# Optimization experiments

Hardware: AMD Instinct MI355X
Metric: run time of the kernel (lower is better)

The kernel has to match this reference:

```python
import jax, jax.numpy as jnp
import numpy as np

N_NODES, N_EDGES, F_IN, F_OUT = 10000, 320000, 256, 256


def setup_inputs() -> dict:
    key = jax.random.key(0)
    k1, k2, k3, k4, k5, k6 = jax.random.split(key, 6)
    feature = jax.random.normal(k1, (N_NODES, F_IN), jnp.float32)
    ew = jax.random.uniform(k2, (N_EDGES,), jnp.float32)          # edge weights
    src = jax.random.randint(k3, (N_EDGES,), 0, N_NODES)
    dst = jax.random.randint(k4, (N_EDGES,), 0, N_NODES)
    # nn.Linear(2*in_feats, out_feats): weight [out, 2*in], bias [out]
    W = jax.random.normal(k5, (F_OUT, 2 * F_IN), jnp.float32) / np.sqrt(2 * F_IN)
    b = jax.random.normal(k6, (F_OUT,), jnp.float32) * 0.01
    return {"feature": feature, "ew": ew, "src": src, "dst": dst, "W": W, "b": b}


def reference(feature, ew, src, dst, W, b):
    n = feature.shape[0]
    # edge_msg2: m[e] = h[src[0]] * h[src[e]] * w[e]   -> [E, F]
    msg = feature[src[0]] * feature[src] * ew[:, None]
    # reduce: segment mean over incoming edges (mailbox mean). The original
    # reduce also computes a segment max concatenated into 'hm', but the apply
    # module only consumes the mean half ('hm_mean', Linear in = 2*in_feats),
    # so the max is dead compute and omitted.
    sums = jax.ops.segment_sum(msg, dst, num_segments=n)
    cnt = jax.ops.segment_sum(jnp.ones((msg.shape[0],), msg.dtype), dst, num_segments=n)
    hm_mean = sums / jnp.maximum(cnt, 1.0)[:, None]
    # NodeApplyModule: relu(Linear(cat(h, hm_mean)))
    x = jnp.concatenate([feature, hm_mean], axis=1)  # [N, 2F]
    return jax.nn.relu(x @ W.T + b)
```

## Files before the change

### kernel.cpp

```cpp
#include <hip/hip_runtime.h>

#define N_NODES 10000
#define N_EDGES 320000
#define F 256
#define K2 512
#define HSLOT 48
#define SLOTS 96
#define CSTR 16
#define W_BLOCKS 128
#define ZCNT_BLOCKS 313
#define K0_BLOCKS (W_BLOCKS + ZCNT_BLOCKS)
#define K1_BLOCKS 4375
#define N_TILE16 625

typedef __attribute__((ext_vector_type(8))) __bf16 bf16x8;
typedef __attribute__((ext_vector_type(4))) __bf16 bf16x4;
typedef __attribute__((ext_vector_type(4))) float f32x4;
typedef __attribute__((ext_vector_type(2))) float f32x2;
typedef unsigned long long u64;
typedef unsigned int u32;
typedef unsigned short u16;


__global__ __launch_bounds__(256) void prep_kernel(
    const float* __restrict__ feat,
    const float* __restrict__ Wm,
    const int* __restrict__ src,
    __bf16* __restrict__ Wt,
    int* __restrict__ cnt) {
  int b = blockIdx.x;
  int tid = threadIdx.x;
  if (b < W_BLOCKS) {
    int idx = b * 256 + tid;
    int o_ = idx >> 7;
    int k = (idx & 127) * 4;
    float4 w = ((const float4*)Wm)[idx];
    if (k >= F) {
      int s0 = src[0];
      float4 h = ((const float4*)(feat + (size_t)s0 * F))[(k - F) >> 2];
      w.x *= h.x; w.y *= h.y; w.z *= h.z; w.w *= h.w;
    }
    bf16x4 o;
    o[0] = (__bf16)w.x; o[1] = (__bf16)w.y; o[2] = (__bf16)w.z; o[3] = (__bf16)w.w;
    int t = k >> 5, kq = (k & 31) >> 3, e = k & 7;
    size_t offT = (((size_t)t * 4 + kq) * 256 + o_) * 8 + e;
    *(bf16x4*)(Wt + offT) = o;
  } else {
    int idx = (b - W_BLOCKS) * 256 + tid;
    if (idx < 2 * N_NODES * CSTR / 4) ((int4*)cnt)[idx] = make_int4(0, 0, 0, 0);
  }
}

__global__ __launch_bounds__(256) void mega_kernel(
    const float* __restrict__ feat,
    const int* __restrict__ src,
    const int* __restrict__ dst,
    const float* __restrict__ ew,
    int* __restrict__ cnt,
    u32* __restrict__ bucket,
    u32* __restrict__ feat8,
    const __bf16* __restrict__ Wt,
    const float* __restrict__ bias,
    float* __restrict__ out) {
  int b = blockIdx.x;
  int tid = threadIdx.x;
  int g = b / 7;
  int r = b % 7;
  if (r == 0 || r == 3) {
    int sid = g * 2 + (r == 3);
    int e = sid * 256 + tid;
    if (e >= N_EDGES) return;
    int d = dst[e];
    int par = e & 1;
    u32 wb = (__float_as_uint(ew[e]) + 0x8000u) & 0xFFFF0000u;
    int p = atomicAdd(&cnt[(d * 2 + par) * CSTR], 1);
    if (p < HSLOT) bucket[(size_t)d * SLOTS + par * HSLOT + p] = wb | (u32)src[e];
  } else if (r == 6) {
    int mt = g;
    const int wave = tid >> 6;
    const int lane = tid & 63;
    const int r15 = lane & 15;
    const int kq = lane >> 4;
    const int col0 = wave * 64;
    const int m0 = mt * 16;
    const float* arow = feat + (size_t)(m0 + r15) * F;

    f32x4 acc[4];
#pragma unroll
    for (int cs = 0; cs < 4; ++cs) acc[cs] = (f32x4){0.f, 0.f, 0.f, 0.f};

#pragma unroll
    for (int t = 0; t < 8; ++t) {
      float4 lo = *(const float4*)(arow + t * 32 + kq * 8);
      float4 hi = *(const float4*)(arow + t * 32 + kq * 8 + 4);
      bf16x8 a;
      a[0] = (__bf16)lo.x; a[1] = (__bf16)lo.y; a[2] = (__bf16)lo.z; a[3] = (__bf16)lo.w;
      a[4] = (__bf16)hi.x; a[5] = (__bf16)hi.y; a[6] = (__bf16)hi.z; a[7] = (__bf16)hi.w;
#pragma unroll
      for (int cs = 0; cs < 4; ++cs) {
        bf16x8 bb = *(const bf16x8*)(Wt + (((size_t)t * 4 + kq) * 256 + col0 + cs * 16 + r15) * 8);
        acc[cs] = __builtin_amdgcn_mfma_f32_16x16x32_bf16(a, bb, acc[cs], 0, 0, 0);
      }
    }

    const int rbase = kq * 4;
#pragma unroll
    for (int cs = 0; cs < 4; ++cs) {
      int col = col0 + cs * 16 + r15;
      float bv = bias[col];
#pragma unroll
      for (int r2 = 0; r2 < 4; ++r2) {
        int orow = m0 + rbase + r2;
        out[(size_t)orow * F + col] = acc[cs][r2] + bv;
      }
    }
  } else {
    int ci = (r < 3) ? (r - 1) : (r - 2);
    int idx = (g * 4 + ci) * 256 + tid;
    float4 v = ((const float4*)feat)[idx];
    u32 r8 = 0;
    r8 = __builtin_amdgcn_cvt_pk_fp8_f32(v.x, v.y, r8, false);
    r8 = __builtin_amdgcn_cvt_pk_fp8_f32(v.z, v.w, r8, true);
    feat8[idx] = r8;
  }
}

__global__ __launch_bounds__(256) void node_agg_kernel(
    const u32* __restrict__ feat8,
    const u32* __restrict__ bucket,
    const int* __restrict__ cnt,
    __bf16* __restrict__ aggb) {
  int node = (blockIdx.x * 256 + threadIdx.x) >> 6;
  int lane = threadIdx.x & 63;
  if (node >= N_NODES) return;
  int c0 = cnt[(node * 2) * CSTR];
  int c1 = cnt[(node * 2 + 1) * CSTR];
  int cc0 = min(c0, HSLOT);
  int cc1 = min(c1, HSLOT);
  int cc = cc0 + cc1;
  int c = c0 + c1;
  const u32* bk = bucket + (size_t)node * SLOTS;
  const uint2* frow = (const uint2*)feat8;
  const int half = lane >> 5;
  const int slot = lane & 31;

  float acc[8];
#pragma unroll
  for (int e = 0; e < 8; ++e) acc[e] = 0.f;

  for (int i = 0; i < cc; i += 16) {
    u32 p[8];
    uint2 v[8];
#pragma unroll
    for (int j = 0; j < 8; ++j) {
      int e = i + half + 2 * j;
      int ec = min(e, cc - 1);
      int si = (ec < cc0) ? ec : (ec - cc0 + HSLOT);
      p[j] = bk[si];
    }
#pragma unroll
    for (int j = 0; j < 8; ++j)
      v[j] = frow[(size_t)(p[j] & 0xFFFFu) * 32 + slot];
#pragma unroll
    for (int j = 0; j < 8; ++j) {
      int e = i + half + 2 * j;
      float w = (e < cc) ? __uint_as_float(p[j] & 0xFFFF0000u) : 0.f;
      f32x2 f01 = __builtin_amdgcn_cvt_pk_f32_fp8(v[j].x, false);
      f32x2 f23 = __builtin_amdgcn_cvt_pk_f32_fp8(v[j].x, true);
      f32x2 f45 = __builtin_amdgcn_cvt_pk_f32_fp8(v[j].y, false);
      f32x2 f67 = __builtin_amdgcn_cvt_pk_f32_fp8(v[j].y, true);
      acc[0] += f01[0] * w; acc[1] += f01[1] * w;
      acc[2] += f23[0] * w; acc[3] += f23[1] * w;
      acc[4] += f45[0] * w; acc[5] += f45[1] * w;
      acc[6] += f67[0] * w; acc[7] += f67[1] * w;
    }
  }

#pragma unroll
  for (int e = 0; e < 8; ++e) acc[e] += __shfl_xor(acc[e], 32, 64);

  if (half == 0) {
    float ic = 1.0f / (float)max(c, 1);
    bf16x8 o;
#pragma unroll
    for (int e = 0; e < 8; ++e) o[e] = (__bf16)(acc[e] * ic);
    *(bf16x8*)(aggb + (size_t)node * F + slot * 8) = o;
  }
}

__global__ __launch_bounds__(256) void gemmB_kernel(
    const __bf16* __restrict__ aggb,
    const __bf16* __restrict__ Wt,
    float* __restrict__ out) {
  const int tid = threadIdx.x;
  const int wave = tid >> 6;
  const int lane = tid & 63;
  const int r15 = lane & 15;
  const int kq = lane >> 4;
  const int col0 = wave * 64;
  const int m0 = blockIdx.x * 16;

  const __bf16* arow = aggb + (size_t)(m0 + r15) * F;

  f32x4 acc[4];
#pragma unroll
  for (int cs = 0; cs < 4; ++cs) acc[cs] = (f32x4){0.f, 0.f, 0.f, 0.f};

#pragma unroll
  for (int t2 = 0; t2 < 8; ++t2) {
    bf16x8 a = *(const bf16x8*)(arow + t2 * 32 + kq * 8);
#pragma unroll
    for (int cs = 0; cs < 4; ++cs) {
      bf16x8 bb = *(const bf16x8*)(Wt + (((size_t)(t2 + 8) * 4 + kq) * 256 + col0 + cs * 16 + r15) * 8);
      acc[cs] = __builtin_amdgcn_mfma_f32_16x16x32_bf16(a, bb, acc[cs], 0, 0, 0);
    }
  }

  const int rbase = kq * 4;
#pragma unroll
  for (int cs = 0; cs < 4; ++cs) {
    int col = col0 + cs * 16 + r15;
#pragma unroll
    for (int r = 0; r < 4; ++r) {
      int orow = m0 + rbase + r;
      size_t oi = (size_t)orow * F + col;
      out[oi] = fmaxf(out[oi] + acc[cs][r], 0.0f);
    }
  }
}

extern "C" void kernel_launch(void* const* d_in, const int* in_sizes, int n_in,
                              void* d_out, int out_size, void* d_ws, size_t ws_size,
                              hipStream_t stream) {
  const float* feat = (const float*)d_in[0];
  const float* ew   = (const float*)d_in[1];
  const int*   src  = (const int*)d_in[2];
  const int*   dst  = (const int*)d_in[3];
  const float* Wm   = (const float*)d_in[4];
  const float* bias = (const float*)d_in[5];
  float* out = (float*)d_out;

  u32*    bucket = (u32*)d_ws;
  __bf16* aggb   = (__bf16*)(bucket + (size_t)N_NODES * SLOTS);
  __bf16* Wt     = aggb + (size_t)N_NODES * F;
  u32*    feat8  = (u32*)(Wt + (size_t)F * K2);
  int*    cnt    = (int*)(feat8 + (size_t)N_NODES * F / 4);

  prep_kernel<<<K0_BLOCKS, 256, 0, stream>>>(feat, Wm, src, Wt, cnt);
  mega_kernel<<<K1_BLOCKS, 256, 0, stream>>>(feat, src, dst, ew, cnt, bucket,
                                             feat8, Wt, bias, out);
  node_agg_kernel<<<(N_NODES * 64 + 255) / 256, 256, 0, stream>>>(feat8, bucket, cnt, aggb);
  gemmB_kernel<<<N_TILE16, 256, 0, stream>>>(aggb, Wt, out);
}
```

Before: 54.50 us.

## Fuse node aggregation into second GEMM via shared-memory tile

Merges the per-node gather/mean kernel with the second-half GEMM: each block aggregates its 16 nodes (4 per wave) into an LDS tile, then runs the MFMA GEMM directly from LDS. This removes one kernel launch and the global round trip of the bf16 aggregate buffer. In exchange, the aggregation now runs on only 625 blocks with each wave handling 4 nodes serially, which lowers parallelism and latency hiding for the gather phase.

```diff
diff --git a/kernel.cpp b/kernel.cpp
--- a/kernel.cpp
+++ b/kernel.cpp
@@ -12,6 +12,7 @@
 #define K0_BLOCKS (W_BLOCKS + ZCNT_BLOCKS)
 #define K1_BLOCKS 4375
 #define N_TILE16 625
+#define LDSROW 264
 
 typedef __attribute__((ext_vector_type(8))) __bf16 bf16x8;
 typedef __attribute__((ext_vector_type(4))) __bf16 bf16x4;
@@ -125,82 +126,80 @@
   }
 }
 
-__global__ __launch_bounds__(256) void node_agg_kernel(
+__global__ __launch_bounds__(256) void aggB_kernel(
     const u32* __restrict__ feat8,
     const u32* __restrict__ bucket,
     const int* __restrict__ cnt,
-    __bf16* __restrict__ aggb) {
-  int node = (blockIdx.x * 256 + threadIdx.x) >> 6;
-  int lane = threadIdx.x & 63;
-  if (node >= N_NODES) return;
-  int c0 = cnt[(node * 2) * CSTR];
-  int c1 = cnt[(node * 2 + 1) * CSTR];
-  int cc0 = min(c0, HSLOT);
-  int cc1 = min(c1, HSLOT);
-  int cc = cc0 + cc1;
-  int c = c0 + c1;
-  const u32* bk = bucket + (size_t)node * SLOTS;
+    const __bf16* __restrict__ Wt,
+    float* __restrict__ out) {
+  __shared__ __bf16 aggs[16][LDSROW];
+
+  const int tid = threadIdx.x;
+  const int wave = tid >> 6;
+  const int lane = tid & 63;
+  const int m0 = blockIdx.x * 16;
+
   const uint2* frow = (const uint2*)feat8;
   const int half = lane >> 5;
   const int slot = lane & 31;
-
-  float acc[8];
-#pragma unroll
-  for (int e = 0; e < 8; ++e) acc[e] = 0.f;
-
-  for (int i = 0; i < cc; i += 16) {
-    u32 p[8];
-    uint2 v[8];
-#pragma unroll
-    for (int j = 0; j < 8; ++j) {
-      int e = i + half + 2 * j;
-      int ec = min(e, cc - 1);
-      int si = (ec < cc0) ? ec : (ec - cc0 + HSLOT);
-      p[j] = bk[si];
-    }
-#pragma unroll
-    for (int j = 0; j < 8; ++j)
-      v[j] = frow[(size_t)(p[j] & 0xFFFFu) * 32 + slot];
-#pragma unroll
-    for (int j = 0; j < 8; ++j) {
-      int e = i + half + 2 * j;
-      float w = (e < cc) ? __uint_as_float(p[j] & 0xFFFF0000u) : 0.f;
-      f32x2 f01 = __builtin_amdgcn_cvt_pk_f32_fp8(v[j].x, false);
-      f32x2 f23 = __builtin_amdgcn_cvt_pk_f32_fp8(v[j].x, true);
-      f32x2 f45 = __builtin_amdgcn_cvt_pk_f32_fp8(v[j].y, false);
-      f32x2 f67 = __builtin_amdgcn_cvt_pk_f32_fp8(v[j].y, true);
-      acc[0] += f01[0] * w; acc[1] += f01[1] * w;
-      acc[2] += f23[0] * w; acc[3] += f23[1] * w;
-      acc[4] += f45[0] * w; acc[5] += f45[1] * w;
-      acc[6] += f67[0] * w; acc[7] += f67[1] * w;
-    }
-  }
-
-#pragma unroll
-  for (int e = 0; e < 8; ++e) acc[e] += __shfl_xor(acc[e], 32, 64);
-
-  if (half == 0) {
-    float ic = 1.0f / (float)max(c, 1);
-    bf16x8 o;
-#pragma unroll
-    for (int e = 0; e < 8; ++e) o[e] = (__bf16)(acc[e] * ic);
-    *(bf16x8*)(aggb + (size_t)node * F + slot * 8) = o;
-  }
-}
-
-__global__ __launch_bounds__(256) void gemmB_kernel(
-    const __bf16* __restrict__ aggb,
-    const __bf16* __restrict__ Wt,
-    float* __restrict__ out) {
-  const int tid = threadIdx.x;
-  const int wave = tid >> 6;
-  const int lane = tid & 63;
+  for (int j = 0; j < 4; ++j) {
+    int node = m0 + wave * 4 + j;
+    int c0 = cnt[(node * 2) * CSTR];
+    int c1 = cnt[(node * 2 + 1) * CSTR];
+    int cc0 = min(c0, HSLOT);
+    int cc1 = min(c1, HSLOT);
+    int cc = cc0 + cc1;
+    int c = c0 + c1;
+    const u32* bk = bucket + (size_t)node * SLOTS;
+
+    float acc[8];
+#pragma unroll
+    for (int e = 0; e < 8; ++e) acc[e] = 0.f;
+
+    for (int i = 0; i < cc; i += 16) {
+      u32 p[8];
+      uint2 v[8];
+#pragma unroll
+      for (int jj = 0; jj < 8; ++jj) {
+        int e = i + half + 2 * jj;
+        int ec = min(e, cc - 1);
+        int si = (ec < cc0) ? ec : (ec - cc0 + HSLOT);
+        p[jj] = bk[si];
+      }
+#pragma unroll
+      for (int jj = 0; jj < 8; ++jj)
+        v[jj] = frow[(size_t)(p[jj] & 0xFFFFu) * 32 + slot];
+#pragma unroll
+      for (int jj = 0; jj < 8; ++jj) {
+        int e = i + half + 2 * jj;
+        float w = (e < cc) ? __uint_as_float(p[jj] & 0xFFFF0000u) : 0.f;
+        f32x2 f01 = __builtin_amdgcn_cvt_pk_f32_fp8(v[jj].x, false);
+        f32x2 f23 = __builtin_amdgcn_cvt_pk_f32_fp8(v[jj].x, true);
+        f32x2 f45 = __builtin_amdgcn_cvt_pk_f32_fp8(v[jj].y, false);
+        f32x2 f67 = __builtin_amdgcn_cvt_pk_f32_fp8(v[jj].y, true);
+        acc[0] += f01[0] * w; acc[1] += f01[1] * w;
+        acc[2] += f23[0] * w; acc[3] += f23[1] * w;
+        acc[4] += f45[0] * w; acc[5] += f45[1] * w;
+        acc[6] += f67[0] * w; acc[7] += f67[1] * w;
+      }
+    }
+
+#pragma unroll
+    for (int e = 0; e < 8; ++e) acc[e] += __shfl_xor(acc[e], 32, 64);
+
+    if (half == 0) {
+      float ic = 1.0f / (float)max(c, 1);
+      bf16x8 o;
+#pragma unroll
+      for (int e = 0; e < 8; ++e) o[e] = (__bf16)(acc[e] * ic);
+      *(bf16x8*)(&aggs[wave * 4 + j][slot * 8]) = o;
+    }
+  }
+  __syncthreads();
+
   const int r15 = lane & 15;
   const int kq = lane >> 4;
   const int col0 = wave * 64;
-  const int m0 = blockIdx.x * 16;
-
-  const __bf16* arow = aggb + (size_t)(m0 + r15) * F;
 
   f32x4 acc[4];
 #pragma unroll
@@ -208,7 +207,7 @@
 
 #pragma unroll
   for (int t2 = 0; t2 < 8; ++t2) {
-    bf16x8 a = *(const bf16x8*)(arow + t2 * 32 + kq * 8);
+    bf16x8 a = *(const bf16x8*)(&aggs[r15][t2 * 32 + kq * 8]);
 #pragma unroll
     for (int cs = 0; cs < 4; ++cs) {
       bf16x8 bb = *(const bf16x8*)(Wt + (((size_t)(t2 + 8) * 4 + kq) * 256 + col0 + cs * 16 + r15) * 8);
@@ -241,14 +240,12 @@
   float* out = (float*)d_out;
 
   u32*    bucket = (u32*)d_ws;
-  __bf16* aggb   = (__bf16*)(bucket + (size_t)N_NODES * SLOTS);
-  __bf16* Wt     = aggb + (size_t)N_NODES * F;
+  __bf16* Wt     = (__bf16*)(bucket + (size_t)N_NODES * SLOTS);
   u32*    feat8  = (u32*)(Wt + (size_t)F * K2);
   int*    cnt    = (int*)(feat8 + (size_t)N_NODES * F / 4);
 
   prep_kernel<<<K0_BLOCKS, 256, 0, stream>>>(feat, Wm, src, Wt, cnt);
   mega_kernel<<<K1_BLOCKS, 256, 0, stream>>>(feat, src, dst, ew, cnt, bucket,
                                              feat8, Wt, bias, out);
-  node_agg_kernel<<<(N_NODES * 64 + 255) / 256, 256, 0, stream>>>(feat8, bucket, cnt, aggb);
-  gemmB_kernel<<<N_TILE16, 256, 0, stream>>>(aggb, Wt, out);
-}
+  aggB_kernel<<<N_TILE16, 256, 0, stream>>>(feat8, bucket, cnt, Wt, out);
+}
```

New measurement: 54.75 us. Within noise of the previous version (+0.4%).
